# Kernel tuning notes

Measured on AMD Instinct MI355X. Metric: run time of the kernel, lower is better.

The kernel has to match this reference:

```python
import jax, jax.numpy as jnp
import numpy as np

D_MODEL = 1024
N_HEAD = 16
D_HEAD = D_MODEL // N_HEAD


def setup_inputs() -> dict:
    key = jax.random.key(0)
    k_x, k_wqkv, k_bqkv, k_wp, k_bp = jax.random.split(key, 5)
    B, T = 2, 2048
    bound = 1.0 / np.sqrt(D_MODEL)
    return {
        "x": jax.random.normal(k_x, (B, T, D_MODEL), dtype=jnp.float32),
        "w_qkv": jax.random.uniform(k_wqkv, (D_MODEL, 3 * D_MODEL), jnp.float32, -bound, bound),
        "b_qkv": jax.random.uniform(k_bqkv, (3 * D_MODEL,), jnp.float32, -bound, bound),
        "w_proj": jax.random.uniform(k_wp, (D_MODEL, D_MODEL), jnp.float32, -bound, bound),
        "b_proj": jax.random.uniform(k_bp, (D_MODEL,), jnp.float32, -bound, bound),
    }


def reference(x, w_qkv, b_qkv, w_proj, b_proj):
    B, T, C = x.shape
    qkv = x @ w_qkv + b_qkv                       # [B,T,3C]
    qkv = qkv.reshape(B, T, 3, N_HEAD, D_HEAD)
    qkv = jnp.transpose(qkv, (2, 0, 3, 1, 4))      # [3,B,H,T,dh]
    q, k, v = qkv[0], qkv[1], qkv[2]
    scale = np.sqrt(D_HEAD).astype(np.float32)
    attn = jnp.einsum("bhqd,bhkd->bhqk", q, k) / scale  # [B,H,T,T]
    causal = jnp.tril(jnp.ones((T, T), dtype=bool))
    attn = jnp.where(causal, attn, -jnp.inf)
    attn = jax.nn.softmax(attn, axis=-1)
    out = jnp.einsum("bhqk,bhkd->bhqd", attn, v)   # [B,H,T,dh]
    out = jnp.transpose(out, (0, 2, 1, 3)).reshape(B, T, C)
    return out @ w_proj + b_proj
```

## Files before the change

### kernel.cpp

```cpp
#include <hip/hip_runtime.h>
#include <hip/hip_bf16.h>
#include <math.h>

constexpr int Bb   = 2;
constexpr int T    = 2048;
constexpr int C    = 1024;
constexpr int H    = 16;
constexpr int M    = Bb * T;
constexpr int NQKV = 3 * C;

typedef __attribute__((ext_vector_type(8))) short bf16x8;
typedef __attribute__((ext_vector_type(4))) float f32x4;

__device__ inline short f2bf(float f) {
    __hip_bfloat16 h = __float2bfloat16(f);
    return *reinterpret_cast<short*>(&h);
}

#if __has_builtin(__builtin_amdgcn_exp2f)
#define EXP2(x) __builtin_amdgcn_exp2f(x)
#else
#define EXP2(x) exp2f(x)
#endif

#define GLOBAL_AS __attribute__((address_space(1)))
#define LDS_AS    __attribute__((address_space(3)))

__device__ __forceinline__ void gload_lds16(const short* g, short* s) {
    __builtin_amdgcn_global_load_lds((const GLOBAL_AS void*)g, (LDS_AS void*)s, 16, 0, 0);
}

__device__ __forceinline__ void lds_fence_wave() {
    __asm__ __volatile__("s_waitcnt lgkmcnt(0)" ::: "memory");
}

__global__ __launch_bounds__(256)
void prep_all(const float* __restrict__ x, short* __restrict__ xb,
              const float* __restrict__ w_qkv, short* __restrict__ wqkvt,
              const float* __restrict__ w_proj, short* __restrict__ wprojt)
{
    __shared__ float tile[32][33];
    const int blk = blockIdx.x;
    const int tid = threadIdx.x;

    if (blk < 4096) {
        const int i = blk * 1024 + tid * 4;
        const float4 v = *(const float4*)(x + i);
        short4 s;
        s.x = f2bf(v.x); s.y = f2bf(v.y); s.z = f2bf(v.z); s.w = f2bf(v.w);
        *(short4*)(xb + i) = s;
        return;
    }

    const bool isqkv = (blk < 7168);
    const int bidx = isqkv ? (blk - 4096) : (blk - 7168);
    const int nblk = isqkv ? 96 : 32;
    const int N    = isqkv ? NQKV : C;
    const float* W = isqkv ? w_qkv : w_proj;
    short* Wt      = isqkv ? wqkvt : wprojt;

    const int n0 = (bidx % nblk) * 32, k0 = (bidx / nblk) * 32;
    const int tx = tid & 31, ty = tid >> 5;
#pragma unroll
    for (int i = 0; i < 32; i += 8)
        tile[ty + i][tx] = W[(size_t)(k0 + ty + i) * N + n0 + tx];
    __syncthreads();
#pragma unroll
    for (int i = 0; i < 32; i += 8)
        Wt[(size_t)(n0 + ty + i) * C + k0 + tx] = f2bf(tile[tx][ty + i]);
}

__global__ __launch_bounds__(256)
void gemm_mfma(const short* __restrict__ A, const short* __restrict__ Bt,
               const float* __restrict__ bias, short* __restrict__ outp,
               int Ndim, int Kdim)
{
    __shared__ __align__(16) short As[128 * 32];
    __shared__ __align__(16) short Bs[128 * 32];

    const int tid = threadIdx.x;
    const int w   = tid >> 6;
    const int l   = tid & 63;
    const int lk  = l & 15;
    const int lq  = l >> 4;
    const int m0  = blockIdx.y * 128, n0 = blockIdx.x * 128;
    const int mw  = (w >> 1) * 64, nw = (w & 1) * 64;

    const int srow = w * 16 + (l >> 2);
    const int scol = (l & 3) * 8;
    short* asdst0 = &As[w * 512];
    short* asdst1 = &As[2048 + w * 512];
    short* bsdst0 = &Bs[w * 512];
    short* bsdst1 = &Bs[2048 + w * 512];

    f32x4 acc[4][4];
#pragma unroll
    for (int i = 0; i < 4; ++i)
#pragma unroll
        for (int j = 0; j < 4; ++j) acc[i][j] = (f32x4){0.f, 0.f, 0.f, 0.f};

    for (int k0 = 0; k0 < Kdim; k0 += 32) {
        __syncthreads();
        gload_lds16(A  + (size_t)(m0 + srow)      * Kdim + k0 + scol, asdst0);
        gload_lds16(A  + (size_t)(m0 + 64 + srow) * Kdim + k0 + scol, asdst1);
        gload_lds16(Bt + (size_t)(n0 + srow)      * Kdim + k0 + scol, bsdst0);
        gload_lds16(Bt + (size_t)(n0 + 64 + srow) * Kdim + k0 + scol, bsdst1);
        __syncthreads();

        bf16x8 af[4], bfr[4];
#pragma unroll
        for (int mt = 0; mt < 4; ++mt)
            af[mt] = *(const bf16x8*)&As[(mw + mt * 16 + lk) * 32 + lq * 8];
#pragma unroll
        for (int nt = 0; nt < 4; ++nt)
            bfr[nt] = *(const bf16x8*)&Bs[(nw + nt * 16 + lk) * 32 + lq * 8];
#pragma unroll
        for (int mt = 0; mt < 4; ++mt)
#pragma unroll
            for (int nt = 0; nt < 4; ++nt)
                acc[mt][nt] = __builtin_amdgcn_mfma_f32_16x16x32_bf16(bfr[nt], af[mt], acc[mt][nt], 0, 0, 0);
    }

    float4 bv[4];
#pragma unroll
    for (int nt = 0; nt < 4; ++nt)
        bv[nt] = *(const float4*)(bias + n0 + nw + nt * 16 + lq * 4);
#pragma unroll
    for (int mt = 0; mt < 4; ++mt) {
        short* rowp = outp + (size_t)(m0 + mw + mt * 16 + lk) * Ndim + n0 + nw + lq * 4;
#pragma unroll
        for (int nt = 0; nt < 4; ++nt) {
            short4 pk;
            pk.x = f2bf(acc[mt][nt][0] + bv[nt].x);
            pk.y = f2bf(acc[mt][nt][1] + bv[nt].y);
            pk.z = f2bf(acc[mt][nt][2] + bv[nt].z);
            pk.w = f2bf(acc[mt][nt][3] + bv[nt].w);
            *(short4*)(rowp + nt * 16) = pk;
        }
    }
}

__global__ __launch_bounds__(256)
void gemm_mfma_proj(const short* __restrict__ A, const short* __restrict__ Bt,
                    const float* __restrict__ bias, float* __restrict__ outp,
                    int Ndim, int Kdim)
{
    __shared__ __align__(16) short As[64 * 32];
    __shared__ __align__(16) short Bs[128 * 32];

    const int tid = threadIdx.x;
    const int w   = tid >> 6;
    const int l   = tid & 63;
    const int lk  = l & 15;
    const int lq  = l >> 4;
    const int m0  = blockIdx.y * 64, n0 = blockIdx.x * 128;
    const int mw  = (w & 1) * 32, nw = (w >> 1) * 64;

    const int srow = w * 16 + (l >> 2);
    const int scol = (l & 3) * 8;
    short* asdst  = &As[w * 512];
    short* bsdst0 = &Bs[w * 512];
    short* bsdst1 = &Bs[2048 + w * 512];

    f32x4 acc[2][4];
#pragma unroll
    for (int i = 0; i < 2; ++i)
#pragma unroll
        for (int j = 0; j < 4; ++j) acc[i][j] = (f32x4){0.f, 0.f, 0.f, 0.f};

    for (int k0 = 0; k0 < Kdim; k0 += 32) {
        __syncthreads();
        gload_lds16(A  + (size_t)(m0 + srow)      * Kdim + k0 + scol, asdst);
        gload_lds16(Bt + (size_t)(n0 + srow)      * Kdim + k0 + scol, bsdst0);
        gload_lds16(Bt + (size_t)(n0 + 64 + srow) * Kdim + k0 + scol, bsdst1);
        __syncthreads();

        bf16x8 af[2], bfr[4];
#pragma unroll
        for (int mt = 0; mt < 2; ++mt)
            af[mt] = *(const bf16x8*)&As[(mw + mt * 16 + lk) * 32 + lq * 8];
#pragma unroll
        for (int nt = 0; nt < 4; ++nt)
            bfr[nt] = *(const bf16x8*)&Bs[(nw + nt * 16 + lk) * 32 + lq * 8];
#pragma unroll
        for (int mt = 0; mt < 2; ++mt)
#pragma unroll
            for (int nt = 0; nt < 4; ++nt)
                acc[mt][nt] = __builtin_amdgcn_mfma_f32_16x16x32_bf16(bfr[nt], af[mt], acc[mt][nt], 0, 0, 0);
    }

    float4 bv[4];
#pragma unroll
    for (int nt = 0; nt < 4; ++nt)
        bv[nt] = *(const float4*)(bias + n0 + nw + nt * 16 + lq * 4);
#pragma unroll
    for (int mt = 0; mt < 2; ++mt) {
        float* rowp = outp + (size_t)(m0 + mw + mt * 16 + lk) * Ndim + n0 + nw + lq * 4;
#pragma unroll
        for (int nt = 0; nt < 4; ++nt) {
            float4 v;
            v.x = acc[mt][nt][0] + bv[nt].x;
            v.y = acc[mt][nt][1] + bv[nt].y;
            v.z = acc[mt][nt][2] + bv[nt].z;
            v.w = acc[mt][nt][3] + bv[nt].w;
            *(float4*)(rowp + nt * 16) = v;
        }
    }
}

constexpr int LDV = 136;
constexpr int LDP = 136;
constexpr float SC = 0.18033688f;

__global__ __launch_bounds__(256)
void attn_mfma(const short* __restrict__ qkv, short* __restrict__ att)
{
    __shared__ __align__(16) short Ks[128 * 64];
    __shared__ __align__(16) short Vt[64 * LDV];
    __shared__ __align__(16) short Ps[4][16 * LDP];

    const int idx = blockIdx.x;
    const int xcd = idx & 7;
    const int j   = idx >> 3;
    const int bh  = xcd * 4 + (j & 3);
    const int s   = j >> 2;
    const int qt  = (s < 8)  ? (31 - s)
                  : (s < 16) ? (s - 8)
                  : (s < 24) ? (39 - s)
                  :            (s - 16);
    const int b   = bh >> 4;
    const int h   = bh & 15;
    const int qbase = qt * 64;

    const int tid = threadIdx.x;
    const int w   = tid >> 6;
    const int l   = tid & 63;
    const int lk  = l & 15;
    const int lq  = l >> 4;

    const short* base = qkv + (size_t)b * T * 3072 + h * 64;

    const int q_abs = qbase + w * 16 + lk;
    const short* qp = base + (size_t)q_abs * 3072 + lq * 8;
    const bf16x8 qf0 = *(const bf16x8*)qp;
    const bf16x8 qf1 = *(const bf16x8*)(qp + 32);

    f32x4 acc_o[4];
#pragma unroll
    for (int dt = 0; dt < 4; ++dt) acc_o[dt] = (f32x4){0.f, 0.f, 0.f, 0.f};
    float m_run = -INFINITY;
    float l_run = 0.f;

    const int ksr = l >> 3;
    const int ksc = (l & 7) * 8;

    const int vkg = (tid & 31) * 4;
    const int vd0 = (tid >> 5) * 8;

    const int nkt = (qbase + 64 + 127) >> 7;
#pragma unroll 1
    for (int it = 0; it < nkt; ++it) {
        const int j0 = it * 128;
        __syncthreads();
#pragma unroll
        for (int rr = 0; rr < 4; ++rr) {
            const int g = w * 32 + rr * 8;
            gload_lds16(base + 1024 + (size_t)(j0 + g + ksr) * 3072 + ksc, &Ks[g * 64]);
        }
        {
            const short* vp = base + 2048 + (size_t)(j0 + vkg) * 3072 + vd0;
            bf16x8 vv[4];
#pragma unroll
            for (int kk = 0; kk < 4; ++kk)
                vv[kk] = *(const bf16x8*)(vp + (size_t)kk * 3072);
#pragma unroll
            for (int d = 0; d < 8; ++d) {
                short4 pk;
                pk.x = vv[0][d]; pk.y = vv[1][d]; pk.z = vv[2][d]; pk.w = vv[3][d];
                *(short4*)&Vt[(vd0 + d) * LDV + vkg] = pk;
            }
        }
        __syncthreads();

        f32x4 s4[8];
#pragma unroll
        for (int kt = 0; kt < 8; ++kt) {
            const bf16x8 kf0 = *(const bf16x8*)&Ks[(kt * 16 + lk) * 64 + lq * 8];
            const bf16x8 kf1 = *(const bf16x8*)&Ks[(kt * 16 + lk) * 64 + 32 + lq * 8];
            f32x4 a = (f32x4){0.f, 0.f, 0.f, 0.f};
            a = __builtin_amdgcn_mfma_f32_16x16x32_bf16(kf0, qf0, a, 0, 0, 0);
            a = __builtin_amdgcn_mfma_f32_16x16x32_bf16(kf1, qf1, a, 0, 0, 0);
            s4[kt] = a;
        }

        if (it == nkt - 1) {
#pragma unroll
            for (int kt = 0; kt < 8; ++kt)
#pragma unroll
                for (int r = 0; r < 4; ++r)
                    if (j0 + kt * 16 + lq * 4 + r > q_abs) s4[kt][r] = -1e30f;
        }

        float mx = s4[0][0];
#pragma unroll
        for (int kt = 0; kt < 8; ++kt)
#pragma unroll
            for (int r = 0; r < 4; ++r) mx = fmaxf(mx, s4[kt][r]);
        mx = fmaxf(mx, __shfl_xor(mx, 16));
        mx = fmaxf(mx, __shfl_xor(mx, 32));
        const float mn   = fmaxf(m_run, mx);
        const float corr = EXP2((m_run - mn) * SC);
        m_run = mn;
        const float nmc = -mn * SC;
#pragma unroll
        for (int kt = 0; kt < 8; ++kt)
#pragma unroll
            for (int r = 0; r < 4; ++r)
                s4[kt][r] = EXP2(fmaf(s4[kt][r], SC, nmc));
        float ps = 0.f;
#pragma unroll
        for (int kt = 0; kt < 8; ++kt)
            ps += ((s4[kt][0] + s4[kt][1]) + (s4[kt][2] + s4[kt][3]));
        ps += __shfl_xor(ps, 16);
        ps += __shfl_xor(ps, 32);
        l_run = l_run * corr + ps;

        short* myP = &Ps[w][0];
#pragma unroll
        for (int kt = 0; kt < 8; ++kt) {
            const unsigned int p01 = (unsigned int)(unsigned short)f2bf(s4[kt][0])
                                   | ((unsigned int)(unsigned short)f2bf(s4[kt][1]) << 16);
            const unsigned int p23 = (unsigned int)(unsigned short)f2bf(s4[kt][2])
                                   | ((unsigned int)(unsigned short)f2bf(s4[kt][3]) << 16);
            *(unsigned int*)&myP[lk * LDP + kt * 16 + lq * 4]     = p01;
            *(unsigned int*)&myP[lk * LDP + kt * 16 + lq * 4 + 2] = p23;
        }

        lds_fence_wave();

#pragma unroll
        for (int dt = 0; dt < 4; ++dt)
#pragma unroll
            for (int r = 0; r < 4; ++r) acc_o[dt][r] *= corr;

#pragma unroll
        for (int kc = 0; kc < 4; ++kc) {
            const bf16x8 pf = *(const bf16x8*)&myP[lk * LDP + kc * 32 + lq * 8];
#pragma unroll
            for (int dt = 0; dt < 4; ++dt) {
                const bf16x8 vf = *(const bf16x8*)&Vt[(dt * 16 + lk) * LDV + kc * 32 + lq * 8];
                acc_o[dt] = __builtin_amdgcn_mfma_f32_16x16x32_bf16(vf, pf, acc_o[dt], 0, 0, 0);
            }
        }
    }

    const float inv = 1.f / l_run;
    short* op = att + ((size_t)(b * T + q_abs)) * 1024 + h * 64;
#pragma unroll
    for (int dt = 0; dt < 4; ++dt) {
        short4 pk;
        pk.x = f2bf(acc_o[dt][0] * inv);
        pk.y = f2bf(acc_o[dt][1] * inv);
        pk.z = f2bf(acc_o[dt][2] * inv);
        pk.w = f2bf(acc_o[dt][3] * inv);
        *(short4*)(op + dt * 16 + lq * 4) = pk;
    }
}

extern "C" void kernel_launch(void* const* d_in, const int* in_sizes, int n_in,
                              void* d_out, int out_size, void* d_ws, size_t ws_size,
                              hipStream_t stream)
{
    const float* x      = (const float*)d_in[0];
    const float* w_qkv  = (const float*)d_in[1];
    const float* b_qkv  = (const float*)d_in[2];
    const float* w_proj = (const float*)d_in[3];
    const float* b_proj = (const float*)d_in[4];
    float* out = (float*)d_out;

    short* xb     = (short*)d_ws;
    short* wqkvt  = xb     + (size_t)M * C;
    short* wprojt = wqkvt  + (size_t)NQKV * C;
    short* qkvb   = wprojt + (size_t)C * C;
    short* attb   = qkvb   + (size_t)M * NQKV;

    prep_all<<<8192, 256, 0, stream>>>(x, xb, w_qkv, wqkvt, w_proj, wprojt);
    gemm_mfma<<<dim3(NQKV / 128, M / 128), 256, 0, stream>>>(xb, wqkvt, b_qkv, qkvb, NQKV, C);
    attn_mfma<<<1024, 256, 0, stream>>>(qkvb, attb);
    gemm_mfma_proj<<<dim3(C / 128, M / 64), 256, 0, stream>>>(attb, wprojt, b_proj, out, C, C);
}
```

Before: 197.8 us.

## Keep P in registers via permuted V layout and swizzle K in LDS

```diff
diff --git a/kernel.cpp b/kernel.cpp
--- a/kernel.cpp
+++ b/kernel.cpp
@@ -28,10 +28,6 @@
 
 __device__ __forceinline__ void gload_lds16(const short* g, short* s) {
     __builtin_amdgcn_global_load_lds((const GLOBAL_AS void*)g, (LDS_AS void*)s, 16, 0, 0);
-}
-
-__device__ __forceinline__ void lds_fence_wave() {
-    __asm__ __volatile__("s_waitcnt lgkmcnt(0)" ::: "memory");
 }
 
 __global__ __launch_bounds__(256)
@@ -209,15 +205,13 @@
 }
 
 constexpr int LDV = 136;
-constexpr int LDP = 136;
 constexpr float SC = 0.18033688f;
 
-__global__ __launch_bounds__(256)
+__global__ __launch_bounds__(256, 4)
 void attn_mfma(const short* __restrict__ qkv, short* __restrict__ att)
 {
     __shared__ __align__(16) short Ks[128 * 64];
     __shared__ __align__(16) short Vt[64 * LDV];
-    __shared__ __align__(16) short Ps[4][16 * LDP];
 
     const int idx = blockIdx.x;
     const int xcd = idx & 7;
@@ -251,11 +245,13 @@
     float m_run = -INFINITY;
     float l_run = 0.f;
 
-    const int ksr = l >> 3;
-    const int ksc = (l & 7) * 8;
-
-    const int vkg = (tid & 31) * 4;
-    const int vd0 = (tid >> 5) * 8;
+    const int krow   = l >> 3;
+    const int kcolsw = 8 * ((l & 7) ^ (l >> 3));
+    const int swz    = lk & 7;
+
+    const int kg   = tid & 31;
+    const int vd0  = (tid >> 5) * 8;
+    const int pcol = ((kg & 24) | ((kg & 3) << 1) | ((kg >> 2) & 1)) * 4;
 
     const int nkt = (qbase + 64 + 127) >> 7;
 #pragma unroll 1
@@ -265,10 +261,10 @@
 #pragma unroll
         for (int rr = 0; rr < 4; ++rr) {
             const int g = w * 32 + rr * 8;
-            gload_lds16(base + 1024 + (size_t)(j0 + g + ksr) * 3072 + ksc, &Ks[g * 64]);
+            gload_lds16(base + 1024 + (size_t)(j0 + g + krow) * 3072 + kcolsw, &Ks[g * 64]);
         }
         {
-            const short* vp = base + 2048 + (size_t)(j0 + vkg) * 3072 + vd0;
+            const short* vp = base + 2048 + (size_t)(j0 + kg * 4) * 3072 + vd0;
             bf16x8 vv[4];
 #pragma unroll
             for (int kk = 0; kk < 4; ++kk)
@@ -277,7 +273,7 @@
             for (int d = 0; d < 8; ++d) {
                 short4 pk;
                 pk.x = vv[0][d]; pk.y = vv[1][d]; pk.z = vv[2][d]; pk.w = vv[3][d];
-                *(short4*)&Vt[(vd0 + d) * LDV + vkg] = pk;
+                *(short4*)&Vt[(vd0 + d) * LDV + pcol] = pk;
             }
         }
         __syncthreads();
@@ -285,8 +281,9 @@
         f32x4 s4[8];
 #pragma unroll
         for (int kt = 0; kt < 8; ++kt) {
-            const bf16x8 kf0 = *(const bf16x8*)&Ks[(kt * 16 + lk) * 64 + lq * 8];
-            const bf16x8 kf1 = *(const bf16x8*)&Ks[(kt * 16 + lk) * 64 + 32 + lq * 8];
+            const int row = kt * 16 + lk;
+            const bf16x8 kf0 = *(const bf16x8*)&Ks[row * 64 + 8 * (lq ^ swz)];
+            const bf16x8 kf1 = *(const bf16x8*)&Ks[row * 64 + 8 * ((lq + 4) ^ swz)];
             f32x4 a = (f32x4){0.f, 0.f, 0.f, 0.f};
             a = __builtin_amdgcn_mfma_f32_16x16x32_bf16(kf0, qf0, a, 0, 0, 0);
             a = __builtin_amdgcn_mfma_f32_16x16x32_bf16(kf1, qf1, a, 0, 0, 0);
@@ -325,18 +322,14 @@
         ps += __shfl_xor(ps, 32);
         l_run = l_run * corr + ps;
 
-        short* myP = &Ps[w][0];
+        unsigned int d0[8], d1[8];
 #pragma unroll
         for (int kt = 0; kt < 8; ++kt) {
-            const unsigned int p01 = (unsigned int)(unsigned short)f2bf(s4[kt][0])
-                                   | ((unsigned int)(unsigned short)f2bf(s4[kt][1]) << 16);
-            const unsigned int p23 = (unsigned int)(unsigned short)f2bf(s4[kt][2])
-                                   | ((unsigned int)(unsigned short)f2bf(s4[kt][3]) << 16);
-            *(unsigned int*)&myP[lk * LDP + kt * 16 + lq * 4]     = p01;
-            *(unsigned int*)&myP[lk * LDP + kt * 16 + lq * 4 + 2] = p23;
-        }
-
-        lds_fence_wave();
+            d0[kt] = (unsigned int)(unsigned short)f2bf(s4[kt][0])
+                   | ((unsigned int)(unsigned short)f2bf(s4[kt][1]) << 16);
+            d1[kt] = (unsigned int)(unsigned short)f2bf(s4[kt][2])
+                   | ((unsigned int)(unsigned short)f2bf(s4[kt][3]) << 16);
+        }
 
 #pragma unroll
         for (int dt = 0; dt < 4; ++dt)
@@ -345,7 +338,12 @@
 
 #pragma unroll
         for (int kc = 0; kc < 4; ++kc) {
-            const bf16x8 pf = *(const bf16x8*)&myP[lk * LDP + kc * 32 + lq * 8];
+            union { unsigned int u[4]; bf16x8 v; } up;
+            up.u[0] = d0[kc * 2];
+            up.u[1] = d1[kc * 2];
+            up.u[2] = d0[kc * 2 + 1];
+            up.u[3] = d1[kc * 2 + 1];
+            const bf16x8 pf = up.v;
 #pragma unroll
             for (int dt = 0; dt < 4; ++dt) {
                 const bf16x8 vf = *(const bf16x8*)&Vt[(dt * 16 + lk) * LDV + kc * 32 + lq * 8];
```

Measured after the change: 188.8 us. 1.05x faster.
